# Optimization experiments

Measured on AMD Instinct MI355X. Metric: run time of the kernel, lower is better.

## Reference

```python
import jax, jax.numpy as jnp
import numpy as np

N = 131072          # events
N_OBS = 64          # observables
HID = [512, 512, 512]          # trunk hidden widths
SUB_HID = [512, 256]           # per-pair subnetwork hidden widths
P = 3                          # number of pairings


def _glorot(key, shape):
    fan_in, fan_out = shape[-2], shape[-1]
    lim = np.sqrt(6.0 / (fan_in + fan_out)).astype(np.float32)
    return jax.random.uniform(key, shape, jnp.float32, -lim, lim)


def setup_inputs() -> dict:
    key = jax.random.key(0)
    ks = jax.random.split(key, 16)
    x = jax.random.normal(ks[0], (N, N_OBS), jnp.float32)
    y = jax.random.randint(ks[1], (N,), 0, 3)
    pairs = jnp.array([[0, 1], [0, 2], [1, 2]], dtype=jnp.int32)
    # trunk params
    W0 = _glorot(ks[2], (N_OBS, HID[0])); b0 = jnp.zeros((HID[0],), jnp.float32)
    W1 = _glorot(ks[3], (HID[0], HID[1])); b1 = jnp.zeros((HID[1],), jnp.float32)
    W2 = _glorot(ks[4], (HID[1], HID[2])); b2 = jnp.zeros((HID[2],), jnp.float32)
    # stacked per-pair subnetwork params (all P subnets share shapes)
    SW0 = _glorot(ks[5], (P, HID[2], SUB_HID[0])); Sb0 = jnp.zeros((P, SUB_HID[0]), jnp.float32)
    SW1 = _glorot(ks[6], (P, SUB_HID[0], SUB_HID[1])); Sb1 = jnp.zeros((P, SUB_HID[1]), jnp.float32)
    SW2 = _glorot(ks[7], (P, SUB_HID[1], 1)); Sb2 = jnp.zeros((P, 1), jnp.float32)
    return {"x": x, "y": y, "pairs": pairs,
            "W0": W0, "b0": b0, "W1": W1, "b1": b1, "W2": W2, "b2": b2,
            "SW0": SW0, "Sb0": Sb0, "SW1": SW1, "Sb1": Sb1, "SW2": SW2, "Sb2": Sb2}


def reference(x, y, pairs, W0, b0, W1, b1, W2, b2, SW0, Sb0, SW1, Sb1, SW2, Sb2):
    relu = jax.nn.relu
    # Trunk. Note: in the torch module with dropout_prob>0, the first Linear sits at
    # layer index 1, so the activation is applied to the raw input as well (eval-mode
    # dropout == identity). We reproduce that exactly.
    h = relu(x) @ W0 + b0
    h = relu(h) @ W1 + b1
    repr_ = relu(h) @ W2 + b2                      # [N, HID[-1]]

    # Per-pair membership masks (jit-safe stand-in for the variable-size gather):
    # mask[p, n] = True iff y[n] is one of the two labels of pairing p.
    mask = (y[None, :] == pairs[:, 0:1]) | (y[None, :] == pairs[:, 1:2])  # [P, N] bool

    # Per-pair RatioModel subnetworks, batched over the pair dim.
    # Same activation-before-every-Linear pattern as the trunk (dropout indices).
    hs = jnp.einsum('nd,pdh->pnh', relu(repr_), SW0) + Sb0[:, None, :]
    hs = jnp.einsum('pnh,phk->pnk', relu(hs), SW1) + Sb1[:, None, :]
    logit = jnp.einsum('pnk,pko->pno', relu(hs), SW2) + Sb2[:, None, :]  # [P, N, 1]
    s_hat = jnp.clip(jax.nn.sigmoid(logit[..., 0]), 1e-9, None)          # [P, N]
    r_hat = (1.0 - s_hat) / s_hat                                        # [P, N]

    maskf = mask.astype(s_hat.dtype)
    return repr_, r_hat * maskf, s_hat * maskf, mask
```

## Files before the change

kernel.cpp:

```cpp
#include <hip/hip_runtime.h>
#include <stdint.h>

#define NE 131072
#define SBCH 32768

typedef __attribute__((ext_vector_type(8))) short bf16x8;
typedef __attribute__((ext_vector_type(4))) float f32x4;

static __device__ __forceinline__ unsigned short f2bf(float f) {
  unsigned u = __float_as_uint(f);
  u += 0x7FFF + ((u >> 16) & 1);
  return (unsigned short)(u >> 16);
}
static __device__ __forceinline__ float bf2f(unsigned short h) {
  return __uint_as_float((unsigned)h << 16);
}
static __device__ __forceinline__ void gload_lds16(const void* g, void* l) {
  __builtin_amdgcn_global_load_lds(
      (const __attribute__((address_space(1))) unsigned*)g,
      (__attribute__((address_space(3))) unsigned*)l, 16, 0, 0);
}

__global__ void prep_all(const float* __restrict__ W0, const float* __restrict__ W1,
                         const float* __restrict__ W2, const float* __restrict__ SW0,
                         const float* __restrict__ SW1, const float* __restrict__ SW2,
                         unsigned short* W0t, unsigned short* W1t,
                         unsigned short* W2t, unsigned short* SW0t,
                         unsigned short* SW1t, unsigned short* SW2b,
                         const float4* __restrict__ x, ushort4* __restrict__ xb,
                         const int* __restrict__ y, const int* __restrict__ pairs,
                         int* __restrict__ idxL, int* __restrict__ posA,
                         int* __restrict__ cnts) {
  const int u = blockIdx.y;
  if (u == 12) {
    const int tot = NE * 64 / 4;
    for (int i = blockIdx.x * 256 + threadIdx.x; i < tot; i += 256 * 256) {
      float4 v = x[i];
      ushort4 o;
      o.x = f2bf(fmaxf(v.x, 0.f));
      o.y = f2bf(fmaxf(v.y, 0.f));
      o.z = f2bf(fmaxf(v.z, 0.f));
      o.w = f2bf(fmaxf(v.w, 0.f));
      xb[i] = o;
    }
    return;
  }
  if (u == 13) {
    if (blockIdx.x >= 12) return;
    const int c = blockIdx.x & 3, p = blockIdx.x >> 2;
    const int la = pairs[p * 2], lb = pairs[p * 2 + 1];
    const long r0 = (long)c * SBCH;
    const long cb = r0;
    __shared__ int wbase[4];
    __shared__ int running;
    if (threadIdx.x == 0) running = 0;
    __syncthreads();
    const int lane = threadIdx.x & 63, wv = threadIdx.x >> 6;
    for (int it = 0; it < SBCH / 256; ++it) {
      const int r = it * 256 + threadIdx.x;
      const int yv = y[r0 + r];
      const bool act = (yv == la) || (yv == lb);
      const unsigned long long m = __ballot(act);
      const int rank = __popcll(m & ((1ull << lane) - 1));
      if (lane == 0) wbase[wv] = __popcll(m);
      __syncthreads();
      int wb = 0;
#pragma unroll
      for (int w = 0; w < 4; ++w) wb += (w < wv) ? wbase[w] : 0;
      const int tot = wbase[0] + wbase[1] + wbase[2] + wbase[3];
      if (act) {
        const int posi = running + wb + rank;
        idxL[(long)p * NE + cb + posi] = r;
        posA[(long)p * NE + r0 + r] = (int)(cb + posi);
      } else {
        posA[(long)p * NE + r0 + r] = -1;
      }
      __syncthreads();
      if (threadIdx.x == 0) running += tot;
      __syncthreads();
    }
    const int cnt = running;
    if (threadIdx.x == 0) cnts[c * 3 + p] = cnt;
    const int padded = (cnt + 255) & ~255;
    const int last = (cnt > 0) ? idxL[(long)p * NE + cb + cnt - 1] : 0;
    for (int i = cnt + threadIdx.x; i < padded; i += 256)
      idxL[(long)p * NE + cb + i] = last;
    return;
  }
  __shared__ float tile[32][33];
  const float* src; unsigned short* dst; int K, Nc;
  if (u == 0)      { src = W0;  dst = W0t;  K = 64;  Nc = 512; }
  else if (u == 1) { src = W1;  dst = W1t;  K = 512; Nc = 512; }
  else if (u == 2) { src = W2;  dst = W2t;  K = 512; Nc = 512; }
  else if (u < 6)  { int p = u - 3; src = SW0 + (long)p * 512 * 512; dst = SW0t + (long)p * 512 * 512; K = 512; Nc = 512; }
  else if (u < 9)  { int p = u - 6; src = SW1 + (long)p * 512 * 256; dst = SW1t + (long)p * 256 * 512; K = 512; Nc = 256; }
  else             { int p = u - 9; src = SW2 + (long)p * 256;       dst = SW2b + (long)p * 256;       K = 256; Nc = 1; }
  const int tkn = K >> 5;
  const int tk = blockIdx.x % tkn, tn = blockIdx.x / tkn;
  if (tn >= ((Nc + 31) >> 5)) return;
  const int k0 = tk * 32, n0 = tn * 32;
  const int tx = threadIdx.x & 31, ty = threadIdx.x >> 5;
  if (n0 + tx < Nc)
#pragma unroll
    for (int j = 0; j < 4; ++j)
      tile[ty * 4 + j][tx] = src[(long)(k0 + ty * 4 + j) * Nc + n0 + tx];
  __syncthreads();
#pragma unroll
  for (int j = 0; j < 4; ++j) {
    int n = n0 + ty * 4 + j;
    if (n < Nc) dst[(long)n * K + k0 + tx] = f2bf(tile[tx][ty * 4 + j]);
  }
}

__global__ __launch_bounds__(512, 4) void gemmT(
    const unsigned short* __restrict__ A, long aZ,
    const unsigned short* __restrict__ Bt, long bZ,
    const float* __restrict__ bias, long biasZ,
    float* __restrict__ outF,
    unsigned short* __restrict__ outA, long cZ,
    int K, int Nc,
    const unsigned short* __restrict__ w2, long w2Z, int r0,
    const int* __restrict__ aIdx, long aIdxZ,
    const int* __restrict__ cnts,
    const float* __restrict__ Sb2v, const int* __restrict__ invIdx,
    float* __restrict__ goR, float* __restrict__ goS,
    float* __restrict__ goM) {
  __shared__ unsigned short lds[3 * 12288];
  __shared__ float part[4][128];
  const int z = blockIdx.z;
  const long brow = (long)blockIdx.x * 128;
  int cpz = 0;
  if (cnts) {
    cpz = cnts[z];
    if ((int)brow >= ((cpz + 255) & ~255)) return;
  }
  A += (long)z * aZ;
  Bt += (long)z * bZ;
  bias += (long)z * biasZ;
  if (outA) outA += (long)z * cZ;
  if (w2) w2 += (long)z * w2Z;
  if (aIdx) aIdx += (long)z * aIdxZ;

  const int tid = threadIdx.x, wave = tid >> 6, lane = tid & 63;
  const int wm = wave >> 2, wn = wave & 3;
  const int lr = lane & 15, lh = lane >> 4;
  const int bcol = blockIdx.y * 256;
  const int nk = K >> 5;
  const int axr = (lh ^ ((lr >> 1) & 3)) * 8;

  const int arL = tid >> 2;
  const int arow = aIdx ? aIdx[brow + arL] : (int)(brow + arL);

  f32x4 acc[4][4];
#pragma unroll
  for (int m = 0; m < 4; ++m)
#pragma unroll
    for (int n = 0; n < 4; ++n) acc[m][n] = (f32x4){0.f, 0.f, 0.f, 0.f};

  auto STAGE = [&](int t) {
    if (t >= nk) return;
    unsigned short* dst = &lds[(t % 3) * 12288];
    const int k0 = t << 5;
    {
      const int c = tid;
      const int r = c >> 2;
      const int kc = (c & 3) ^ ((r >> 1) & 3);
      gload_lds16(A + (long)arow * K + k0 + kc * 8, &dst[(wave * 64) * 8]);
    }
#pragma unroll
    for (int i = 0; i < 2; ++i) {
      const int cb = i * 512 + wave * 64;
      const int c = cb + lane;
      const int r = c >> 2;
      const int kc = (c & 3) ^ ((r >> 1) & 3);
      gload_lds16(Bt + (long)(bcol + r) * K + k0 + kc * 8,
                  &dst[(512 + cb) * 8]);
    }
  };

  STAGE(0);
  STAGE(1);

  for (int t = 0; t < nk; ++t) {
    if (t < nk - 1)
      asm volatile("s_waitcnt vmcnt(3)" ::: "memory");
    else
      asm volatile("s_waitcnt vmcnt(0)" ::: "memory");
    __builtin_amdgcn_s_barrier();
    __builtin_amdgcn_sched_barrier(0);
    const unsigned short* buf = &lds[(t % 3) * 12288];
    bf16x8 a[4], b[4];
#pragma unroll
    for (int m = 0; m < 4; ++m)
      a[m] = *(const bf16x8*)&buf[(wm * 64 + m * 16 + lr) * 32 + axr];
#pragma unroll
    for (int n = 0; n < 4; ++n)
      b[n] = *(const bf16x8*)&buf[512 * 8 + (wn * 64 + n * 16 + lr) * 32 + axr];
    STAGE(t + 2);
    __builtin_amdgcn_s_setprio(1);
#pragma unroll
    for (int m = 0; m < 4; ++m)
#pragma unroll
      for (int n = 0; n < 4; ++n)
        acc[m][n] =
            __builtin_amdgcn_mfma_f32_16x16x32_bf16(a[m], b[n], acc[m][n], 0, 0, 0);
    __builtin_amdgcn_s_setprio(0);
  }

  float bv[4];
#pragma unroll
  for (int n = 0; n < 4; ++n) bv[n] = bias[bcol + wn * 64 + n * 16 + lr];

  if (!w2) {
#pragma unroll
    for (int m = 0; m < 4; ++m) {
#pragma unroll
      for (int r = 0; r < 4; ++r) {
        long e = brow + wm * 64 + m * 16 + lh * 4 + r;
#pragma unroll
        for (int n = 0; n < 4; ++n) {
          int oc = bcol + wn * 64 + n * 16 + lr;
          float v = acc[m][n][r] + bv[n];
          if (outF) __builtin_nontemporal_store(v, &outF[e * Nc + oc]);
          if (outA) outA[e * Nc + oc] = f2bf(fmaxf(v, 0.f));
        }
      }
    }
  } else {
    float w2v[4];
#pragma unroll
    for (int n = 0; n < 4; ++n) w2v[n] = bf2f(w2[wn * 64 + n * 16 + lr]);
#pragma unroll
    for (int m = 0; m < 4; ++m) {
#pragma unroll
      for (int r = 0; r < 4; ++r) {
        float s = 0.f;
#pragma unroll
        for (int n = 0; n < 4; ++n)
          s += fmaxf(acc[m][n][r] + bv[n], 0.f) * w2v[n];
#pragma unroll
        for (int off = 1; off < 16; off <<= 1) s += __shfl_xor(s, off);
        if (lr == 0) part[wn][wm * 64 + m * 16 + lh * 4 + r] = s;
      }
    }
    __syncthreads();
    if (tid < 128) {
      const int posL = (int)brow + tid;
      if (posL < cpz) {
        float logit = part[0][tid] + part[1][tid] + part[2][tid] +
                      part[3][tid] + Sb2v[z];
        float s = 1.f / (1.f + expf(-logit));
        s = fmaxf(s, 1e-9f);
        float rr = (1.f - s) / s;
        const long orig = (long)r0 + invIdx[(long)z * NE + r0 + posL];
        goR[(long)z * NE + orig] = rr;
        goS[(long)z * NE + orig] = s;
        goM[(long)z * NE + orig] = 1.f;
      }
    }
  }
}

extern "C" void kernel_launch(void* const* d_in, const int* in_sizes, int n_in,
                              void* d_out, int out_size, void* d_ws, size_t ws_size,
                              hipStream_t stream) {
  const float* x   = (const float*)d_in[0];
  const int*   y   = (const int*)d_in[1];
  const int*   prs = (const int*)d_in[2];
  const float* W0  = (const float*)d_in[3];
  const float* b0  = (const float*)d_in[4];
  const float* W1  = (const float*)d_in[5];
  const float* b1  = (const float*)d_in[6];
  const float* W2  = (const float*)d_in[7];
  const float* b2  = (const float*)d_in[8];
  const float* SW0 = (const float*)d_in[9];
  const float* Sb0 = (const float*)d_in[10];
  const float* SW1 = (const float*)d_in[11];
  const float* Sb1 = (const float*)d_in[12];
  const float* SW2 = (const float*)d_in[13];
  const float* Sb2 = (const float*)d_in[14];

  uint8_t* ws = (uint8_t*)d_ws;
  size_t off = 0;
  auto take = [&](size_t bytes) -> void* {
    void* ptr = ws + off;
    off = (off + bytes + 255) & ~(size_t)255;
    return ptr;
  };
  unsigned short* W0t  = (unsigned short*)take((size_t)64 * 512 * 2);
  unsigned short* W1t  = (unsigned short*)take((size_t)512 * 512 * 2);
  unsigned short* W2t  = (unsigned short*)take((size_t)512 * 512 * 2);
  unsigned short* SW0t = (unsigned short*)take((size_t)3 * 512 * 512 * 2);
  unsigned short* SW1t = (unsigned short*)take((size_t)3 * 256 * 512 * 2);
  unsigned short* SW2b = (unsigned short*)take((size_t)3 * 256 * 2);
  unsigned short* Xb   = (unsigned short*)take((size_t)NE * 64 * 2);
  int*            idxL = (int*)take((size_t)3 * NE * 4);
  int*            posA = (int*)take((size_t)3 * NE * 4);
  int*            cnts = (int*)take((size_t)64 * 4);

  const long chunk = SBCH;
  const int nchunks = (int)(NE / chunk);

  unsigned short* T0   = (unsigned short*)take((size_t)chunk * 512 * 2);
  unsigned short* T1   = (unsigned short*)take((size_t)chunk * 512 * 2);
  unsigned short* bufR = (unsigned short*)take((size_t)chunk * 512 * 2);
  unsigned short* H3   = (unsigned short*)take((size_t)3 * chunk * 512 * 2);

  float* out   = (float*)d_out;
  float* outRe = out;
  float* outR  = out + (size_t)NE * 512;
  float* outS  = outR + (size_t)3 * NE;
  float* outM  = outS + (size_t)3 * NE;

  prep_all<<<dim3(256, 14), 256, 0, stream>>>(
      W0, W1, W2, SW0, SW1, SW2, W0t, W1t, W2t, SW0t, SW1t, SW2b,
      (const float4*)x, (ushort4*)Xb, y, prs, idxL, posA, cnts);
  hipMemsetAsync(outR, 0, (size_t)9 * NE * 4, stream);

  for (int c = 0; c < nchunks; ++c) {
    const long r0 = (long)c * chunk;
    gemmT<<<dim3(chunk / 128, 2, 1), 512, 0, stream>>>(
        Xb + r0 * 64, 0, W0t, 0, b0, 0, nullptr, T0, 0, 64, 512,
        nullptr, 0, 0, nullptr, 0, nullptr,
        nullptr, nullptr, nullptr, nullptr, nullptr);
    gemmT<<<dim3(chunk / 128, 2, 1), 512, 0, stream>>>(
        T0, 0, W1t, 0, b1, 0, nullptr, T1, 0, 512, 512,
        nullptr, 0, 0, nullptr, 0, nullptr,
        nullptr, nullptr, nullptr, nullptr, nullptr);
    gemmT<<<dim3(chunk / 128, 2, 1), 512, 0, stream>>>(
        T1, 0, W2t, 0, b2, 0, outRe + r0 * 512, bufR, 0, 512, 512,
        nullptr, 0, 0, nullptr, 0, nullptr,
        nullptr, nullptr, nullptr, nullptr, nullptr);
    gemmT<<<dim3(chunk / 128, 2, 3), 512, 0, stream>>>(
        bufR, 0, SW0t, (long)512 * 512, Sb0, 512, nullptr,
        H3, (long)chunk * 512, 512, 512,
        nullptr, 0, 0, idxL + r0, NE, cnts + c * 3,
        nullptr, nullptr, nullptr, nullptr, nullptr);
    gemmT<<<dim3(chunk / 128, 1, 3), 512, 0, stream>>>(
        H3, (long)chunk * 512, SW1t, (long)256 * 512, Sb1, 256, nullptr,
        nullptr, 0, 512, 256,
        SW2b, 256, (int)r0, nullptr, 0, cnts + c * 3,
        Sb2, idxL, outR, outS, outM);
  }
}
```

Baseline: 675.9 us.

## Co-schedule GEMM stages from adjacent chunks in merged launches

Generalizes the GEMM kernel to take two argument sets and a flat block index, so one launch can run a stage of chunk c alongside an independent stage of chunk c+1. Trunk intermediate buffers are double-buffered so the interleaved chunks do not collide. This fills the GPU better and removes tail and launch gaps between the per-chunk dependent GEMMs. The cost is extra workspace, a larger kernel-argument struct, and divergent scheduling where blocks of one half may finish early or exit via count checks.

```diff
diff --git a/kernel.cpp b/kernel.cpp
--- a/kernel.cpp
+++ b/kernel.cpp
@@ -112,39 +112,41 @@
   }
 }
 
-__global__ __launch_bounds__(512, 4) void gemmT(
-    const unsigned short* __restrict__ A, long aZ,
-    const unsigned short* __restrict__ Bt, long bZ,
-    const float* __restrict__ bias, long biasZ,
-    float* __restrict__ outF,
-    unsigned short* __restrict__ outA, long cZ,
-    int K, int Nc,
-    const unsigned short* __restrict__ w2, long w2Z, int r0,
-    const int* __restrict__ aIdx, long aIdxZ,
-    const int* __restrict__ cnts,
-    const float* __restrict__ Sb2v, const int* __restrict__ invIdx,
-    float* __restrict__ goR, float* __restrict__ goS,
-    float* __restrict__ goM) {
-  __shared__ unsigned short lds[3 * 12288];
-  __shared__ float part[4][128];
-  const int z = blockIdx.z;
-  const long brow = (long)blockIdx.x * 128;
+struct GArgs {
+  const unsigned short* A; long aZ;
+  const unsigned short* Bt; long bZ;
+  const float* bias; long biasZ;
+  float* outF;
+  unsigned short* outA; long cZ;
+  int K, Nc;
+  const unsigned short* w2; long w2Z; int r0;
+  const int* aIdx; long aIdxZ;
+  const int* cnts;
+  const float* Sb2v; const int* invIdx;
+  float* goR; float* goS; float* goM;
+  int gx, gy, gz;
+};
+
+static __device__ __forceinline__ void gemm_body(
+    unsigned short* lds, float* part, int bx, int by, int z, const GArgs& G) {
+  const long brow = (long)bx * 128;
   int cpz = 0;
-  if (cnts) {
-    cpz = cnts[z];
+  if (G.cnts) {
+    cpz = G.cnts[z];
     if ((int)brow >= ((cpz + 255) & ~255)) return;
   }
-  A += (long)z * aZ;
-  Bt += (long)z * bZ;
-  bias += (long)z * biasZ;
-  if (outA) outA += (long)z * cZ;
-  if (w2) w2 += (long)z * w2Z;
-  if (aIdx) aIdx += (long)z * aIdxZ;
+  const unsigned short* A = G.A + (long)z * G.aZ;
+  const unsigned short* Bt = G.Bt + (long)z * G.bZ;
+  const float* bias = G.bias + (long)z * G.biasZ;
+  unsigned short* outA = G.outA ? G.outA + (long)z * G.cZ : nullptr;
+  const unsigned short* w2 = G.w2 ? G.w2 + (long)z * G.w2Z : nullptr;
+  const int* aIdx = G.aIdx ? G.aIdx + (long)z * G.aIdxZ : nullptr;
+  const int K = G.K, Nc = G.Nc;
 
   const int tid = threadIdx.x, wave = tid >> 6, lane = tid & 63;
   const int wm = wave >> 2, wn = wave & 3;
   const int lr = lane & 15, lh = lane >> 4;
-  const int bcol = blockIdx.y * 256;
+  const int bcol = by * 256;
   const int nk = K >> 5;
   const int axr = (lh ^ ((lr >> 1) & 3)) * 8;
 
@@ -221,7 +223,7 @@
         for (int n = 0; n < 4; ++n) {
           int oc = bcol + wn * 64 + n * 16 + lr;
           float v = acc[m][n][r] + bv[n];
-          if (outF) __builtin_nontemporal_store(v, &outF[e * Nc + oc]);
+          if (G.outF) __builtin_nontemporal_store(v, &G.outF[e * Nc + oc]);
           if (outA) outA[e * Nc + oc] = f2bf(fmaxf(v, 0.f));
         }
       }
@@ -240,24 +242,40 @@
           s += fmaxf(acc[m][n][r] + bv[n], 0.f) * w2v[n];
 #pragma unroll
         for (int off = 1; off < 16; off <<= 1) s += __shfl_xor(s, off);
-        if (lr == 0) part[wn][wm * 64 + m * 16 + lh * 4 + r] = s;
+        if (lr == 0) part[wn * 128 + wm * 64 + m * 16 + lh * 4 + r] = s;
       }
     }
     __syncthreads();
     if (tid < 128) {
       const int posL = (int)brow + tid;
       if (posL < cpz) {
-        float logit = part[0][tid] + part[1][tid] + part[2][tid] +
-                      part[3][tid] + Sb2v[z];
+        float logit = part[tid] + part[128 + tid] + part[256 + tid] +
+                      part[384 + tid] + G.Sb2v[z];
         float s = 1.f / (1.f + expf(-logit));
         s = fmaxf(s, 1e-9f);
         float rr = (1.f - s) / s;
-        const long orig = (long)r0 + invIdx[(long)z * NE + r0 + posL];
-        goR[(long)z * NE + orig] = rr;
-        goS[(long)z * NE + orig] = s;
-        goM[(long)z * NE + orig] = 1.f;
+        const long orig = (long)G.r0 + G.invIdx[(long)z * NE + G.r0 + posL];
+        G.goR[(long)z * NE + orig] = rr;
+        G.goS[(long)z * NE + orig] = s;
+        G.goM[(long)z * NE + orig] = 1.f;
       }
     }
+  }
+}
+
+__global__ __launch_bounds__(512, 4) void gemmT2(GArgs ga, GArgs gb, int nA) {
+  __shared__ unsigned short lds[3 * 12288];
+  __shared__ float part[512];
+  const int bid = blockIdx.x;
+  if (bid < nA) {
+    const int bx = bid % ga.gx;
+    const int t = bid / ga.gx;
+    gemm_body(lds, part, bx, t % ga.gy, t / ga.gy, ga);
+  } else {
+    const int id = bid - nA;
+    const int bx = id % gb.gx;
+    const int t = id / gb.gx;
+    gemm_body(lds, part, bx, t % gb.gy, t / gb.gy, gb);
   }
 }
 
@@ -299,12 +317,13 @@
   int*            cnts = (int*)take((size_t)64 * 4);
 
   const long chunk = SBCH;
-  const int nchunks = (int)(NE / chunk);
-
-  unsigned short* T0   = (unsigned short*)take((size_t)chunk * 512 * 2);
-  unsigned short* T1   = (unsigned short*)take((size_t)chunk * 512 * 2);
-  unsigned short* bufR = (unsigned short*)take((size_t)chunk * 512 * 2);
-  unsigned short* H3   = (unsigned short*)take((size_t)3 * chunk * 512 * 2);
+  unsigned short* T0[2], *T1[2], *bufR[2];
+  for (int i = 0; i < 2; ++i) {
+    T0[i]   = (unsigned short*)take((size_t)chunk * 512 * 2);
+    T1[i]   = (unsigned short*)take((size_t)chunk * 512 * 2);
+    bufR[i] = (unsigned short*)take((size_t)chunk * 512 * 2);
+  }
+  unsigned short* H3 = (unsigned short*)take((size_t)3 * chunk * 512 * 2);
 
   float* out   = (float*)d_out;
   float* outRe = out;
@@ -317,29 +336,68 @@
       (const float4*)x, (ushort4*)Xb, y, prs, idxL, posA, cnts);
   hipMemsetAsync(outR, 0, (size_t)9 * NE * 4, stream);
 
-  for (int c = 0; c < nchunks; ++c) {
-    const long r0 = (long)c * chunk;
-    gemmT<<<dim3(chunk / 128, 2, 1), 512, 0, stream>>>(
-        Xb + r0 * 64, 0, W0t, 0, b0, 0, nullptr, T0, 0, 64, 512,
-        nullptr, 0, 0, nullptr, 0, nullptr,
-        nullptr, nullptr, nullptr, nullptr, nullptr);
-    gemmT<<<dim3(chunk / 128, 2, 1), 512, 0, stream>>>(
-        T0, 0, W1t, 0, b1, 0, nullptr, T1, 0, 512, 512,
-        nullptr, 0, 0, nullptr, 0, nullptr,
-        nullptr, nullptr, nullptr, nullptr, nullptr);
-    gemmT<<<dim3(chunk / 128, 2, 1), 512, 0, stream>>>(
-        T1, 0, W2t, 0, b2, 0, outRe + r0 * 512, bufR, 0, 512, 512,
-        nullptr, 0, 0, nullptr, 0, nullptr,
-        nullptr, nullptr, nullptr, nullptr, nullptr);
-    gemmT<<<dim3(chunk / 128, 2, 3), 512, 0, stream>>>(
-        bufR, 0, SW0t, (long)512 * 512, Sb0, 512, nullptr,
-        H3, (long)chunk * 512, 512, 512,
-        nullptr, 0, 0, idxL + r0, NE, cnts + c * 3,
-        nullptr, nullptr, nullptr, nullptr, nullptr);
-    gemmT<<<dim3(chunk / 128, 1, 3), 512, 0, stream>>>(
-        H3, (long)chunk * 512, SW1t, (long)256 * 512, Sb1, 256, nullptr,
-        nullptr, 0, 512, 256,
-        SW2b, 256, (int)r0, nullptr, 0, cnts + c * 3,
-        Sb2, idxL, outR, outS, outM);
-  }
-}
+  auto base = [&]() {
+    GArgs g{};
+    g.gx = (int)(chunk / 128); g.gy = 2; g.gz = 1;
+    return g;
+  };
+  auto mkL0 = [&](int c) {
+    GArgs g = base();
+    g.A = Xb + (long)c * chunk * 64; g.Bt = W0t; g.bias = b0;
+    g.outA = T0[c & 1]; g.K = 64; g.Nc = 512;
+    return g;
+  };
+  auto mkL1 = [&](int c) {
+    GArgs g = base();
+    g.A = T0[c & 1]; g.Bt = W1t; g.bias = b1;
+    g.outA = T1[c & 1]; g.K = 512; g.Nc = 512;
+    return g;
+  };
+  auto mkL2 = [&](int c) {
+    GArgs g = base();
+    g.A = T1[c & 1]; g.Bt = W2t; g.bias = b2;
+    g.outF = outRe + (long)c * chunk * 512;
+    g.outA = bufR[c & 1]; g.K = 512; g.Nc = 512;
+    return g;
+  };
+  auto mkS0 = [&](int c) {
+    GArgs g = base();
+    g.A = bufR[c & 1]; g.Bt = SW0t; g.bZ = (long)512 * 512;
+    g.bias = Sb0; g.biasZ = 512; g.outA = H3; g.cZ = (long)chunk * 512;
+    g.K = 512; g.Nc = 512;
+    g.aIdx = idxL + (long)c * chunk; g.aIdxZ = NE; g.cnts = cnts + c * 3;
+    g.gz = 3;
+    return g;
+  };
+  auto mkS1 = [&](int c) {
+    GArgs g = base();
+    g.A = H3; g.aZ = (long)chunk * 512; g.Bt = SW1t; g.bZ = (long)256 * 512;
+    g.bias = Sb1; g.biasZ = 256; g.K = 512; g.Nc = 256;
+    g.w2 = SW2b; g.w2Z = 256; g.r0 = (int)((long)c * chunk);
+    g.cnts = cnts + c * 3; g.Sb2v = Sb2; g.invIdx = idxL;
+    g.goR = outR; g.goS = outS; g.goM = outM;
+    g.gy = 1; g.gz = 3;
+    return g;
+  };
+  auto one = [&](GArgs a) {
+    int nA = a.gx * a.gy * a.gz;
+    gemmT2<<<dim3(nA), 512, 0, stream>>>(a, a, nA);
+  };
+  auto two = [&](GArgs a, GArgs b) {
+    int nA = a.gx * a.gy * a.gz, nB = b.gx * b.gy * b.gz;
+    gemmT2<<<dim3(nA + nB), 512, 0, stream>>>(a, b, nA);
+  };
+
+  one(mkL0(0));
+  two(mkL1(0), mkL0(1));
+  two(mkL2(0), mkL1(1));
+  two(mkS0(0), mkL2(1));
+  two(mkS1(0), mkL0(2));
+  two(mkS0(1), mkL1(2));
+  two(mkS1(1), mkL2(2));
+  two(mkS0(2), mkL0(3));
+  two(mkS1(2), mkL1(3));
+  one(mkL2(3));
+  one(mkS0(3));
+  one(mkS1(3));
+}
```

Result: no change. 671.3 us (-0.7%).
